# Kernel optimization log

Measured on AMD Instinct MI355X. Metric: run time of the kernel, lower is better.

The kernel has to match this reference:

```python
import jax, jax.numpy as jnp
import numpy as np

D_MODEL = 1024

def setup_inputs() -> dict:
    key = jax.random.key(0)
    ks = jax.random.split(key, 5)
    s = 1.0 / np.sqrt(D_MODEL)  # torch Linear default init scale-ish
    x = jax.random.normal(ks[0], (4, 2048, D_MODEL), dtype=jnp.float32)
    Wq = jax.random.normal(ks[1], (D_MODEL, D_MODEL), dtype=jnp.float32) * s
    Wk = jax.random.normal(ks[2], (D_MODEL, D_MODEL), dtype=jnp.float32) * s
    Wv = jax.random.normal(ks[3], (D_MODEL, D_MODEL), dtype=jnp.float32) * s
    Wo = jax.random.normal(ks[4], (D_MODEL, D_MODEL), dtype=jnp.float32) * s
    z = jnp.zeros((D_MODEL,), dtype=jnp.float32)
    return {"x": x, "Wq": Wq, "bq": z, "Wk": Wk, "bk": z, "Wv": Wv, "bv": z, "Wo": Wo, "bo": z}

def reference(x, Wq, bq, Wk, bk, Wv, bv, Wo, bo):
    # x: (B, S, D). Single-head causal attention, dropout in eval mode (identity).
    B, S, D = x.shape
    Q = jnp.einsum('bsd,ed->bse', x, Wq) + bq
    K = jnp.einsum('bsd,ed->bse', x, Wk) + bk
    V = jnp.einsum('bsd,ed->bse', x, Wv) + bv
    scores = jnp.einsum('bqd,bkd->bqk', Q, K) / jnp.sqrt(jnp.float32(D))
    causal = jnp.tril(jnp.ones((S, S), dtype=bool))  # (S, S)
    scores = jnp.where(causal, scores, -jnp.inf)
    weights = jax.nn.softmax(scores, axis=-1)
    attended = jnp.einsum('bqk,bkd->bqd', weights, V)
    out = jnp.einsum('bsd,ed->bse', attended, Wo) + bo
    return out
```

## Files before the change

### kernel.cpp

```cpp
#include <hip/hip_runtime.h>
#include <cstdint>
#include <cstddef>


#define D_MODEL 1024
#define SEQ     2048
#define BATCH   4

typedef unsigned short u16;
typedef __bf16 bf16_t;
typedef bf16_t bf16x8 __attribute__((ext_vector_type(8)));
typedef float  f32x4  __attribute__((ext_vector_type(4)));
typedef u16    u16x4  __attribute__((ext_vector_type(4)));

__device__ __forceinline__ u16 f2bf(float x) {
  union { float f; uint32_t u; } v; v.f = x;
  uint32_t r = v.u + 0x7fffu + ((v.u >> 16) & 1u);
  return (u16)(r >> 16);
}
__device__ __forceinline__ float bf2f(u16 h) {
  union { uint32_t u; float f; } v; v.u = (uint32_t)h << 16;
  return v.f;
}

__device__ __forceinline__ void gload_lds16(const u16* g, u16* l) {
  __builtin_amdgcn_global_load_lds((__attribute__((address_space(1))) void*)g,
                                   (__attribute__((address_space(3))) void*)l,
                                   16, 0, 0);
}

__device__ __forceinline__ void gemm256(const u16* __restrict__ A,
                                        const u16* __restrict__ B,
                                        int lda, int ldb, int nt64,
                                        u16* As, u16* Bs,
                                        f32x4 acc[8][4]) {
  const int tid  = threadIdx.x;
  const int lane = tid & 63, wave = tid >> 6;
  const int frow = lane & 15, kc = lane >> 4;
  const int abase = (wave >> 2) * 128, bbase = (wave & 3) * 64;
  const int r0 = tid >> 2;
  const int k0 = ((tid & 3) ^ ((r0 >> 1) & 3)) * 8;
  const u16* Arow0 = A + (size_t)r0 * lda + k0;
  const u16* Arow1 = A + (size_t)(r0 + 128) * lda + k0;
  const u16* Brow0 = B + (size_t)r0 * ldb + k0;
  const u16* Brow1 = B + (size_t)(r0 + 128) * ldb + k0;
  int aoff[8], boff[4];
#pragma unroll
  for (int i = 0; i < 8; ++i) {
    const int ra = abase + i * 16 + frow;
    aoff[i] = (ra * 4 + (kc ^ ((ra >> 1) & 3))) * 8;
  }
#pragma unroll
  for (int j = 0; j < 4; ++j) {
    const int rb = bbase + j * 16 + frow;
    boff[j] = (rb * 4 + (kc ^ ((rb >> 1) & 3))) * 8;
  }
  auto stage = [&](int t) {
    u16* ab = As + (t & 1) * 16384;
    u16* bb = Bs + (t & 1) * 16384;
    const int kb = t * 64;
    gload_lds16(Arow0 + kb,      ab + tid * 8);
    gload_lds16(Arow1 + kb,      ab + 4096 + tid * 8);
    gload_lds16(Arow0 + kb + 32, ab + 8192 + tid * 8);
    gload_lds16(Arow1 + kb + 32, ab + 12288 + tid * 8);
    gload_lds16(Brow0 + kb,      bb + tid * 8);
    gload_lds16(Brow1 + kb,      bb + 4096 + tid * 8);
    gload_lds16(Brow0 + kb + 32, bb + 8192 + tid * 8);
    gload_lds16(Brow1 + kb + 32, bb + 12288 + tid * 8);
  };
  stage(0);
  for (int t = 0; t < nt64; ++t) {
    __builtin_amdgcn_s_barrier();
    if (t + 1 < nt64) {
      stage(t + 1);
      asm volatile("s_waitcnt vmcnt(8)" ::: "memory");
    } else {
      asm volatile("s_waitcnt vmcnt(0)" ::: "memory");
    }
    __builtin_amdgcn_s_barrier();
    const u16* ab = As + (t & 1) * 16384;
    const u16* bb = Bs + (t & 1) * 16384;
    bf16x8 a0[4], a1[4], b0[4], b1[4];
#pragma unroll
    for (int j = 0; j < 4; ++j) b0[j] = *(const bf16x8*)(bb + boff[j]);
#pragma unroll
    for (int i = 0; i < 4; ++i) a0[i] = *(const bf16x8*)(ab + aoff[i]);
#pragma unroll
    for (int i = 0; i < 4; ++i) a1[i] = *(const bf16x8*)(ab + aoff[4 + i]);
    __builtin_amdgcn_s_setprio(1);
#pragma unroll
    for (int i = 0; i < 4; ++i)
#pragma unroll
      for (int j = 0; j < 4; ++j)
        acc[i][j] = __builtin_amdgcn_mfma_f32_16x16x32_bf16(a0[i], b0[j], acc[i][j], 0, 0, 0);
    __builtin_amdgcn_s_setprio(0);
#pragma unroll
    for (int j = 0; j < 4; ++j) b1[j] = *(const bf16x8*)(bb + 8192 + boff[j]);
#pragma unroll
    for (int i = 0; i < 4; ++i) a0[i] = *(const bf16x8*)(ab + 8192 + aoff[i]);
    __builtin_amdgcn_s_setprio(1);
#pragma unroll
    for (int i = 0; i < 4; ++i)
#pragma unroll
      for (int j = 0; j < 4; ++j)
        acc[4 + i][j] = __builtin_amdgcn_mfma_f32_16x16x32_bf16(a1[i], b0[j], acc[4 + i][j], 0, 0, 0);
    __builtin_amdgcn_s_setprio(0);
#pragma unroll
    for (int i = 0; i < 4; ++i) a1[i] = *(const bf16x8*)(ab + 8192 + aoff[4 + i]);
    __builtin_amdgcn_s_setprio(1);
#pragma unroll
    for (int i = 0; i < 4; ++i)
#pragma unroll
      for (int j = 0; j < 4; ++j)
        acc[i][j] = __builtin_amdgcn_mfma_f32_16x16x32_bf16(a0[i], b1[j], acc[i][j], 0, 0, 0);
#pragma unroll
    for (int i = 0; i < 4; ++i)
#pragma unroll
      for (int j = 0; j < 4; ++j)
        acc[4 + i][j] = __builtin_amdgcn_mfma_f32_16x16x32_bf16(a1[i], b1[j], acc[4 + i][j], 0, 0, 0);
    __builtin_amdgcn_s_setprio(0);
  }
}

__device__ __forceinline__ void gemm128(const u16* __restrict__ A,
                                        const u16* __restrict__ B,
                                        int lda, int ldb, int nt,
                                        u16* As, u16* Bs,
                                        f32x4 acc[4][2]) {
  const int tid  = threadIdx.x;
  const int lane = tid & 63, wave = tid >> 6;
  const int frow = lane & 15, kc = lane >> 4;
  const int abase = (wave >> 2) * 64, bbase = (wave & 3) * 32;
  const int r0 = tid >> 2;
  const int k0 = ((tid & 3) ^ ((r0 >> 1) & 3)) * 8;
  const u16* Asrc = A + (size_t)r0 * lda + k0;
  const u16* Bsrc = B + (size_t)r0 * ldb + k0;
  int aoff[4], boff[2];
#pragma unroll
  for (int i = 0; i < 4; ++i) {
    const int ra = abase + i * 16 + frow;
    aoff[i] = (ra * 4 + (kc ^ ((ra >> 1) & 3))) * 8;
  }
#pragma unroll
  for (int j = 0; j < 2; ++j) {
    const int rb = bbase + j * 16 + frow;
    boff[j] = (rb * 4 + (kc ^ ((rb >> 1) & 3))) * 8;
  }
  auto stage = [&](int t) {
    u16* ab = As + (t & 3) * 4096;
    u16* bb = Bs + (t & 3) * 4096;
    const int kb = t * 32;
    gload_lds16(Asrc + kb, ab + tid * 8);
    gload_lds16(Bsrc + kb, bb + tid * 8);
  };
  stage(0);
  if (nt > 1) stage(1);
  if (nt > 2) stage(2);
  for (int t = 0; t < nt; ++t) {
    if (t + 2 < nt)      asm volatile("s_waitcnt vmcnt(4)" ::: "memory");
    else if (t + 1 < nt) asm volatile("s_waitcnt vmcnt(2)" ::: "memory");
    else                 asm volatile("s_waitcnt vmcnt(0)" ::: "memory");
    __builtin_amdgcn_s_barrier();
    asm volatile("" ::: "memory");
    if (t + 3 < nt) stage(t + 3);
    const u16* ab = As + (t & 3) * 4096;
    const u16* bb = Bs + (t & 3) * 4096;
    bf16x8 af[4], bf[2];
#pragma unroll
    for (int j = 0; j < 2; ++j) bf[j] = *(const bf16x8*)(bb + boff[j]);
#pragma unroll
    for (int i = 0; i < 4; ++i) af[i] = *(const bf16x8*)(ab + aoff[i]);
    __builtin_amdgcn_s_setprio(1);
#pragma unroll
    for (int i = 0; i < 4; ++i)
#pragma unroll
      for (int j = 0; j < 2; ++j)
        acc[i][j] = __builtin_amdgcn_mfma_f32_16x16x32_bf16(af[i], bf[j], acc[i][j], 0, 0, 0);
    __builtin_amdgcn_s_setprio(0);
    asm volatile("" ::: "memory");
  }
}

__global__ __launch_bounds__(256) void cvt_kernel(const float4* __restrict__ x,
                                                  const float4* __restrict__ wq,
                                                  const float4* __restrict__ wk,
                                                  const float4* __restrict__ wv,
                                                  const float4* __restrict__ wo,
                                                  u16* __restrict__ dst) {
  const int i = blockIdx.x * 256 + threadIdx.x;
  float4 v;
  if (i < 2097152) {
    v = x[i];
  } else {
    const int j = i - 2097152;
    const int w = j >> 18;
    const float4* s = (w == 0) ? wq : (w == 1) ? wk : (w == 2) ? wv : wo;
    v = s[j & 262143];
  }
  u16x4 o = {f2bf(v.x), f2bf(v.y), f2bf(v.z), f2bf(v.w)};
  *(u16x4*)(dst + (size_t)i * 4) = o;
}

__global__ void transposeW_kernel(const u16* __restrict__ src, u16* __restrict__ dst) {
  __shared__ u16 tile[32][33];
  const int r0 = blockIdx.x * 32, c0 = blockIdx.y * 32;
  const int tx = threadIdx.x, ty = threadIdx.y;
#pragma unroll
  for (int r = 0; r < 4; ++r)
    tile[ty + r * 8][tx] = src[(size_t)(r0 + ty + r * 8) * D_MODEL + c0 + tx];
  __syncthreads();
#pragma unroll
  for (int r = 0; r < 4; ++r)
    dst[(size_t)(c0 + ty + r * 8) * D_MODEL + r0 + tx] = tile[tx][ty + r * 8];
}

__global__ __launch_bounds__(512, 2) void stageA_kernel(
    const u16* __restrict__ xb,
    const u16* __restrict__ WqB, const u16* __restrict__ WkB,
    const u16* __restrict__ WoB, const u16* __restrict__ WvT,
    const float* __restrict__ Wo32, const float* __restrict__ bv,
    const float* __restrict__ bq, const float* __restrict__ bk,
    u16* __restrict__ Qb, u16* __restrict__ Kb,
    u16* __restrict__ Wp, float* __restrict__ bp) {
  __shared__ __align__(16) u16 As[32768];
  __shared__ __align__(16) u16 Bs[32768];
  const int blk = blockIdx.x, tid = threadIdx.x;
  const int lane = tid & 63, wave = tid >> 6;
  const int cl = lane & 15, rl = (lane >> 4) * 4;

  if (blk < 256) {
    const int c = blk & 7, i = blk >> 3;
    const int z = i >> 4, w = i & 15;
    const int rt = c * 4 + (w >> 2), ct = w & 3;
    const int row0 = rt * 256, col0 = ct * 256;
    const u16*   W    = z ? WkB : WqB;
    const float* bias = z ? bk : bq;
    u16*         out  = z ? Kb : Qb;
    f32x4 acc[8][4] = {};
    gemm256(xb + (size_t)row0 * D_MODEL, W + (size_t)col0 * D_MODEL,
            D_MODEL, D_MODEL, 16, As, Bs, acc);
    const int abase = (wave >> 2) * 128, bbase = (wave & 3) * 64;
#pragma unroll
    for (int j = 0; j < 4; ++j) {
      const int col = col0 + bbase + j * 16 + cl;
      const float bb = bias[col];
#pragma unroll
      for (int ii = 0; ii < 8; ++ii)
#pragma unroll
        for (int r = 0; r < 4; ++r) {
          const int row = row0 + abase + ii * 16 + rl + r;
          out[(size_t)row * D_MODEL + col] = f2bf(acc[ii][j][r] + bb);
        }
    }
  } else if (blk < 320) {
    const int qq = blk - 256;
    const int t16 = qq >> 2, quad = qq & 3;
    const int f0 = (t16 >> 2) * 256 + (quad >> 1) * 128;
    const int e0 = (t16 & 3) * 256 + (quad & 1) * 128;
    f32x4 acc[4][2] = {};
    gemm128(WoB + (size_t)f0 * D_MODEL, WvT + (size_t)e0 * D_MODEL,
            D_MODEL, D_MODEL, 32, As, Bs, acc);
    const int abase = (wave >> 2) * 64, bbase = (wave & 3) * 32;
#pragma unroll
    for (int j = 0; j < 2; ++j) {
      const int col = e0 + bbase + j * 16 + cl;
#pragma unroll
      for (int ii = 0; ii < 4; ++ii)
#pragma unroll
        for (int r = 0; r < 4; ++r) {
          const int row = f0 + abase + ii * 16 + rl + r;
          Wp[(size_t)row * D_MODEL + col] = f2bf(acc[ii][j][r]);
        }
    }
  } else {
    const int f  = (blk - 320) * 64 + (tid >> 3);
    const int dq = tid & 7;
    const float* row = Wo32 + (size_t)f * D_MODEL + dq * 128;
    const float* bvq = bv + dq * 128;
    float s = 0.f;
#pragma unroll 8
    for (int k = 0; k < 128; ++k) s += row[k] * bvq[k];
    s += __shfl_xor(s, 1);
    s += __shfl_xor(s, 2);
    s += __shfl_xor(s, 4);
    if (dq == 0) bp[f] = s;
  }
}

__global__ __launch_bounds__(512, 2) void stageB_kernel(
    const u16* __restrict__ xb, const u16* __restrict__ Wp,
    const float* __restrict__ bp,
    const u16* __restrict__ Qb, const u16* __restrict__ Kb,
    u16* __restrict__ Vt, u16* __restrict__ Eb, float* __restrict__ rssum) {
  __shared__ __align__(16) u16 As[32768];
  __shared__ __align__(16) u16 Bs[32768];
  const int blk = blockIdx.x, tid = threadIdx.x;
  const int lane = tid & 63, wave = tid >> 6;
  const int cl = lane & 15, rl = (lane >> 4) * 4;

  if (blk < 144) {
    const int c = blk & 7, u = blk >> 3;
    const int b = c >> 1, h = c & 1;
    int qi, ji;
    if (h == 0) {
      if (u < 1)       { qi = 0; ji = u; }
      else if (u < 5)  { qi = 3; ji = u - 1; }
      else if (u < 10) { qi = 4; ji = u - 5; }
      else             { qi = 7; ji = u - 10; }
    } else {
      if (u < 2)       { qi = 1; ji = u; }
      else if (u < 5)  { qi = 2; ji = u - 2; }
      else if (u < 11) { qi = 5; ji = u - 5; }
      else             { qi = 6; ji = u - 11; }
    }
    const u16* A  = Qb + (size_t)(b * SEQ + qi * 256) * D_MODEL;
    const u16* Bt = Kb + (size_t)(b * SEQ + ji * 256) * D_MODEL;
    f32x4 acc[8][4] = {};
    gemm256(A, Bt, D_MODEL, D_MODEL, 16, As, Bs, acc);
    u16* outp = Eb + (size_t)b * SEQ * SEQ;
    float* rs = rssum + b * SEQ;
    const int abase = (wave >> 2) * 128, bbase = (wave & 3) * 64;
#pragma unroll
    for (int ii = 0; ii < 8; ++ii)
#pragma unroll
      for (int r = 0; r < 4; ++r) {
        const int q = qi * 256 + abase + ii * 16 + rl + r;
        float ps = 0.f;
#pragma unroll
        for (int j = 0; j < 4; ++j) {
          const int jj = ji * 256 + bbase + j * 16 + cl;
          u16 h16 = 0;
          if (jj <= q) h16 = f2bf(__expf(acc[ii][j][r] * 0.03125f));
          outp[(size_t)q * SEQ + jj] = h16;
          ps += bf2f(h16);
        }
        ps += __shfl_xor(ps, 1);
        ps += __shfl_xor(ps, 2);
        ps += __shfl_xor(ps, 4);
        ps += __shfl_xor(ps, 8);
        if (cl == 0) atomicAdd(&rs[q], ps);
      }
  } else if (blk < 256) {
    const int v = blk - 144;
    const int rt = v >> 2, ct = v & 3;
    const int row0 = rt * 256, col0 = ct * 256;
    f32x4 acc[8][4] = {};
    gemm256(xb + (size_t)row0 * D_MODEL, Wp + (size_t)col0 * D_MODEL,
            D_MODEL, D_MODEL, 16, As, Bs, acc);
    const int b = row0 >> 11;
    u16* vt = Vt + (size_t)b * D_MODEL * SEQ;
    const int abase = (wave >> 2) * 128, bbase = (wave & 3) * 64;
#pragma unroll
    for (int j = 0; j < 4; ++j) {
      const int col = col0 + bbase + j * 16 + cl;
      const float bb = bp[col];
#pragma unroll
      for (int ii = 0; ii < 8; ++ii) {
        const int s0 = (row0 & 2047) + abase + ii * 16 + rl;
        u16x4 o = {f2bf(acc[ii][j][0] + bb), f2bf(acc[ii][j][1] + bb),
                   f2bf(acc[ii][j][2] + bb), f2bf(acc[ii][j][3] + bb)};
        *(u16x4*)(vt + (size_t)col * SEQ + s0) = o;
      }
    }
  } else {
    const int qq = blk - 256;
    const int t16 = qq >> 2, quad = qq & 3;
    const int rt = 28 + (t16 >> 2), ct = t16 & 3;
    const int row0 = rt * 256 + (quad >> 1) * 128;
    const int col0 = ct * 256 + (quad & 1) * 128;
    f32x4 acc[4][2] = {};
    gemm128(xb + (size_t)row0 * D_MODEL, Wp + (size_t)col0 * D_MODEL,
            D_MODEL, D_MODEL, 32, As, Bs, acc);
    const int b = row0 >> 11;
    u16* vt = Vt + (size_t)b * D_MODEL * SEQ;
    const int abase = (wave >> 2) * 64, bbase = (wave & 3) * 32;
#pragma unroll
    for (int j = 0; j < 2; ++j) {
      const int col = col0 + bbase + j * 16 + cl;
      const float bb = bp[col];
#pragma unroll
      for (int ii = 0; ii < 4; ++ii) {
        const int s0 = (row0 & 2047) + abase + ii * 16 + rl;
        u16x4 o = {f2bf(acc[ii][j][0] + bb), f2bf(acc[ii][j][1] + bb),
                   f2bf(acc[ii][j][2] + bb), f2bf(acc[ii][j][3] + bb)};
        *(u16x4*)(vt + (size_t)col * SEQ + s0) = o;
      }
    }
  }
}

__global__ __launch_bounds__(512, 2) void pv_kernel(const u16* __restrict__ Eb,
                                                    const u16* __restrict__ Vt,
                                                    const float* __restrict__ rssum,
                                                    const float* __restrict__ bo,
                                                    float* __restrict__ Out) {
  __shared__ __align__(16) u16 As[32768];
  __shared__ __align__(16) u16 Bs[32768];
  const int blk = blockIdx.x, tid = threadIdx.x;
  const int c = blk & 7, i = blk >> 3;
  const int b  = c >> 1;
  const int dt = (c & 1) * 2 + (i & 1);
  const int qt = i >> 1;
  const u16* A  = Eb + (size_t)b * SEQ * SEQ + (size_t)(qt * 256) * SEQ;
  const u16* Bt = Vt + (size_t)b * D_MODEL * SEQ + (size_t)(dt * 256) * SEQ;
  f32x4 acc[8][4] = {};
  gemm256(A, Bt, SEQ, SEQ, (qt + 1) * 4, As, Bs, acc);
  const int lane = tid & 63, wave = tid >> 6;
  const int abase = (wave >> 2) * 128, bbase = (wave & 3) * 64;
  const int cl = lane & 15, rl = (lane >> 4) * 4;
#pragma unroll
  for (int ii = 0; ii < 8; ++ii)
#pragma unroll
    for (int r = 0; r < 4; ++r) {
      const int q = qt * 256 + abase + ii * 16 + rl + r;
      const float invl = 1.0f / rssum[b * SEQ + q];
#pragma unroll
      for (int j = 0; j < 4; ++j) {
        const int col = dt * 256 + bbase + j * 16 + cl;
        Out[(size_t)(b * SEQ + q) * D_MODEL + col] = acc[ii][j][r] * invl + bo[col];
      }
    }
}

extern "C" void kernel_launch(void* const* d_in, const int* in_sizes, int n_in,
                              void* d_out, int out_size, void* d_ws, size_t ws_size,
                              hipStream_t stream) {
  const float* x  = (const float*)d_in[0];
  const float* Wq = (const float*)d_in[1];
  const float* bq = (const float*)d_in[2];
  const float* Wk = (const float*)d_in[3];
  const float* bk = (const float*)d_in[4];
  const float* Wv = (const float*)d_in[5];
  const float* bv = (const float*)d_in[6];
  const float* Wo = (const float*)d_in[7];
  const float* bo = (const float*)d_in[8];
  float* out = (float*)d_out;
  char* ws = (char*)d_ws;

  u16*   xb  = (u16*)(ws);
  u16*   Wb  = (u16*)(ws + (16u << 20));
  u16*   Qb  = (u16*)(ws + (24u << 20));
  u16*   Kb  = (u16*)(ws + (40u << 20));
  u16*   Vt  = (u16*)(ws + (56u << 20));
  u16*   Eb  = (u16*)(ws + (72u << 20));
  u16*   WvT = (u16*)(ws + (104u << 20));
  u16*   Wp  = (u16*)(ws + (106u << 20));
  float* bp  = (float*)(ws + (108u << 20));
  float* rssum = (float*)(ws + (20u << 20));

  cvt_kernel<<<12288, 256, 0, stream>>>((const float4*)x, (const float4*)Wq,
                                        (const float4*)Wk, (const float4*)Wv,
                                        (const float4*)Wo, xb);
  transposeW_kernel<<<dim3(32, 32), dim3(32, 8), 0, stream>>>(Wb + (2u << 20), WvT);
  stageA_kernel<<<336, 512, 0, stream>>>(xb, Wb, Wb + (1u << 20), Wb + (3u << 20),
                                         WvT, Wo, bv, bq, bk, Qb, Kb, Wp, bp);
  hipMemsetAsync(rssum, 0, BATCH * SEQ * sizeof(float), stream);
  stageB_kernel<<<320, 512, 0, stream>>>(xb, Wp, bp, Qb, Kb, Vt, Eb, rssum);
  pv_kernel<<<128, 512, 0, stream>>>(Eb, Vt, rssum, bo, out);
}
```

Baseline: 292.3 us.

## Deepen gemm pipeline to 4-stage half-K ring and rebalance PV with paired causal tiles

The shared gemm256 loop moves from a double-buffered 64-wide K step to a 4-deep ring of 32-wide K stages. Loads for stage h+3 are issued between the LDS fragment reads and the MFMAs, and vmcnt waits are tracked per stage, so global latency is hidden further ahead. The PV kernel now uses a new 128x128 gemm with the same ring and 256 blocks. Each block handles a pair of causal query tiles (q and 15-q), giving every block the same total work and filling more CUs. The cost is more barriers per K step and smaller tiles with less operand reuse.

After: 254.3 us. 1.15x faster.

```diff
diff --git a/kernel.cpp b/kernel.cpp
--- a/kernel.cpp
+++ b/kernel.cpp
@@ -55,70 +55,131 @@
     const int rb = bbase + j * 16 + frow;
     boff[j] = (rb * 4 + (kc ^ ((rb >> 1) & 3))) * 8;
   }
-  auto stage = [&](int t) {
-    u16* ab = As + (t & 1) * 16384;
-    u16* bb = Bs + (t & 1) * 16384;
-    const int kb = t * 64;
-    gload_lds16(Arow0 + kb,      ab + tid * 8);
-    gload_lds16(Arow1 + kb,      ab + 4096 + tid * 8);
-    gload_lds16(Arow0 + kb + 32, ab + 8192 + tid * 8);
-    gload_lds16(Arow1 + kb + 32, ab + 12288 + tid * 8);
-    gload_lds16(Brow0 + kb,      bb + tid * 8);
-    gload_lds16(Brow1 + kb,      bb + 4096 + tid * 8);
-    gload_lds16(Brow0 + kb + 32, bb + 8192 + tid * 8);
-    gload_lds16(Brow1 + kb + 32, bb + 12288 + tid * 8);
+  const int H = nt64 * 2;
+  auto stgA = [&](int hh) {
+    const int koff = hh * 32;
+    u16* ab = As + (hh & 3) * 8192;
+    gload_lds16(Arow0 + koff, ab + tid * 8);
+    gload_lds16(Arow1 + koff, ab + 4096 + tid * 8);
   };
-  stage(0);
-  for (int t = 0; t < nt64; ++t) {
-    __builtin_amdgcn_s_barrier();
-    if (t + 1 < nt64) {
-      stage(t + 1);
-      asm volatile("s_waitcnt vmcnt(8)" ::: "memory");
-    } else {
-      asm volatile("s_waitcnt vmcnt(0)" ::: "memory");
-    }
-    __builtin_amdgcn_s_barrier();
-    const u16* ab = As + (t & 1) * 16384;
-    const u16* bb = Bs + (t & 1) * 16384;
-    bf16x8 a0[4], a1[4], b0[4], b1[4];
-#pragma unroll
-    for (int j = 0; j < 4; ++j) b0[j] = *(const bf16x8*)(bb + boff[j]);
-#pragma unroll
-    for (int i = 0; i < 4; ++i) a0[i] = *(const bf16x8*)(ab + aoff[i]);
-#pragma unroll
-    for (int i = 0; i < 4; ++i) a1[i] = *(const bf16x8*)(ab + aoff[4 + i]);
+  auto stgB = [&](int hh) {
+    const int koff = hh * 32;
+    u16* bb = Bs + (hh & 3) * 8192;
+    gload_lds16(Brow0 + koff, bb + tid * 8);
+    gload_lds16(Brow1 + koff, bb + 4096 + tid * 8);
+  };
+  stgA(0); stgB(0);
+  if (H > 1) { stgA(1); stgB(1); }
+  if (H > 2) { stgA(2); stgB(2); }
+  if (H > 2)      asm volatile("s_waitcnt vmcnt(8)" ::: "memory");
+  else if (H > 1) asm volatile("s_waitcnt vmcnt(4)" ::: "memory");
+  else            asm volatile("s_waitcnt vmcnt(0)" ::: "memory");
+  __builtin_amdgcn_s_barrier();
+  for (int h = 0; h < H; ++h) {
+    const u16* ab = As + (h & 3) * 8192;
+    const u16* bb = Bs + (h & 3) * 8192;
+    bf16x8 bf[4], af[4];
+#pragma unroll
+    for (int j = 0; j < 4; ++j) bf[j] = *(const bf16x8*)(bb + boff[j]);
+#pragma unroll
+    for (int i = 0; i < 4; ++i) af[i] = *(const bf16x8*)(ab + aoff[i]);
+    if (h + 3 < H) stgA(h + 3);
+    __builtin_amdgcn_s_barrier();
+    asm volatile("s_waitcnt lgkmcnt(0)" ::: "memory");
+    __builtin_amdgcn_sched_barrier(0);
     __builtin_amdgcn_s_setprio(1);
 #pragma unroll
     for (int i = 0; i < 4; ++i)
 #pragma unroll
       for (int j = 0; j < 4; ++j)
-        acc[i][j] = __builtin_amdgcn_mfma_f32_16x16x32_bf16(a0[i], b0[j], acc[i][j], 0, 0, 0);
+        acc[i][j] = __builtin_amdgcn_mfma_f32_16x16x32_bf16(af[i], bf[j], acc[i][j], 0, 0, 0);
     __builtin_amdgcn_s_setprio(0);
-#pragma unroll
-    for (int j = 0; j < 4; ++j) b1[j] = *(const bf16x8*)(bb + 8192 + boff[j]);
-#pragma unroll
-    for (int i = 0; i < 4; ++i) a0[i] = *(const bf16x8*)(ab + 8192 + aoff[i]);
+    __builtin_amdgcn_s_barrier();
+#pragma unroll
+    for (int i = 0; i < 4; ++i) af[i] = *(const bf16x8*)(ab + aoff[4 + i]);
+    if (h + 3 < H) stgB(h + 3);
+    __builtin_amdgcn_s_barrier();
+    asm volatile("s_waitcnt lgkmcnt(0)" ::: "memory");
+    __builtin_amdgcn_sched_barrier(0);
     __builtin_amdgcn_s_setprio(1);
 #pragma unroll
     for (int i = 0; i < 4; ++i)
 #pragma unroll
       for (int j = 0; j < 4; ++j)
-        acc[4 + i][j] = __builtin_amdgcn_mfma_f32_16x16x32_bf16(a1[i], b0[j], acc[4 + i][j], 0, 0, 0);
+        acc[4 + i][j] = __builtin_amdgcn_mfma_f32_16x16x32_bf16(af[i], bf[j], acc[4 + i][j], 0, 0, 0);
     __builtin_amdgcn_s_setprio(0);
-#pragma unroll
-    for (int i = 0; i < 4; ++i) a1[i] = *(const bf16x8*)(ab + 8192 + aoff[4 + i]);
+    if (h + 1 < H) {
+      const int infl = H - 2 - h;
+      if (infl >= 2)      asm volatile("s_waitcnt vmcnt(8)" ::: "memory");
+      else if (infl == 1) asm volatile("s_waitcnt vmcnt(4)" ::: "memory");
+      else                asm volatile("s_waitcnt vmcnt(0)" ::: "memory");
+    }
+    __builtin_amdgcn_s_barrier();
+  }
+}
+
+__device__ __forceinline__ void gemm128pv(const u16* __restrict__ A,
+                                          const u16* __restrict__ B,
+                                          int lda, int ldb, int H,
+                                          u16* As, u16* Bs,
+                                          f32x4 acc[4][2]) {
+  const int tid  = threadIdx.x;
+  const int lane = tid & 63, wave = tid >> 6;
+  const int frow = lane & 15, kc = lane >> 4;
+  const int abase = (wave >> 2) * 64, bbase = (wave & 3) * 32;
+  const int r0 = tid >> 2;
+  const int k0 = ((tid & 3) ^ ((r0 >> 1) & 3)) * 8;
+  const u16* Asrc = A + (size_t)r0 * lda + k0;
+  const u16* Bsrc = B + (size_t)r0 * ldb + k0;
+  int aoff[4], boff[2];
+#pragma unroll
+  for (int i = 0; i < 4; ++i) {
+    const int ra = abase + i * 16 + frow;
+    aoff[i] = (ra * 4 + (kc ^ ((ra >> 1) & 3))) * 8;
+  }
+#pragma unroll
+  for (int j = 0; j < 2; ++j) {
+    const int rb = bbase + j * 16 + frow;
+    boff[j] = (rb * 4 + (kc ^ ((rb >> 1) & 3))) * 8;
+  }
+  auto stg = [&](int hh) {
+    const int koff = hh * 32;
+    gload_lds16(Asrc + koff, As + (hh & 3) * 4096 + tid * 8);
+    gload_lds16(Bsrc + koff, Bs + (hh & 3) * 4096 + tid * 8);
+  };
+  stg(0);
+  if (H > 1) stg(1);
+  if (H > 2) stg(2);
+  if (H > 2)      asm volatile("s_waitcnt vmcnt(4)" ::: "memory");
+  else if (H > 1) asm volatile("s_waitcnt vmcnt(2)" ::: "memory");
+  else            asm volatile("s_waitcnt vmcnt(0)" ::: "memory");
+  __builtin_amdgcn_s_barrier();
+  for (int h = 0; h < H; ++h) {
+    const u16* ab = As + (h & 3) * 4096;
+    const u16* bb = Bs + (h & 3) * 4096;
+    bf16x8 af[4], bf[2];
+#pragma unroll
+    for (int j = 0; j < 2; ++j) bf[j] = *(const bf16x8*)(bb + boff[j]);
+#pragma unroll
+    for (int i = 0; i < 4; ++i) af[i] = *(const bf16x8*)(ab + aoff[i]);
+    if (h + 3 < H) stg(h + 3);
+    __builtin_amdgcn_s_barrier();
+    asm volatile("s_waitcnt lgkmcnt(0)" ::: "memory");
+    __builtin_amdgcn_sched_barrier(0);
     __builtin_amdgcn_s_setprio(1);
 #pragma unroll
     for (int i = 0; i < 4; ++i)
 #pragma unroll
-      for (int j = 0; j < 4; ++j)
-        acc[i][j] = __builtin_amdgcn_mfma_f32_16x16x32_bf16(a0[i], b1[j], acc[i][j], 0, 0, 0);
-#pragma unroll
-    for (int i = 0; i < 4; ++i)
-#pragma unroll
-      for (int j = 0; j < 4; ++j)
-        acc[4 + i][j] = __builtin_amdgcn_mfma_f32_16x16x32_bf16(a1[i], b1[j], acc[4 + i][j], 0, 0, 0);
+      for (int j = 0; j < 2; ++j)
+        acc[i][j] = __builtin_amdgcn_mfma_f32_16x16x32_bf16(af[i], bf[j], acc[i][j], 0, 0, 0);
     __builtin_amdgcn_s_setprio(0);
+    if (h + 1 < H) {
+      const int infl = H - 2 - h;
+      if (infl >= 2)      asm volatile("s_waitcnt vmcnt(4)" ::: "memory");
+      else if (infl == 1) asm volatile("s_waitcnt vmcnt(2)" ::: "memory");
+      else                asm volatile("s_waitcnt vmcnt(0)" ::: "memory");
+    }
+    __builtin_amdgcn_s_barrier();
   }
 }
 
@@ -394,32 +455,37 @@
                                                     const float* __restrict__ rssum,
                                                     const float* __restrict__ bo,
                                                     float* __restrict__ Out) {
-  __shared__ __align__(16) u16 As[32768];
-  __shared__ __align__(16) u16 Bs[32768];
+  __shared__ __align__(16) u16 As[16384];
+  __shared__ __align__(16) u16 Bs[16384];
   const int blk = blockIdx.x, tid = threadIdx.x;
-  const int c = blk & 7, i = blk >> 3;
+  const int c = blk & 7, s = blk >> 3;
   const int b  = c >> 1;
-  const int dt = (c & 1) * 2 + (i & 1);
-  const int qt = i >> 1;
-  const u16* A  = Eb + (size_t)b * SEQ * SEQ + (size_t)(qt * 256) * SEQ;
-  const u16* Bt = Vt + (size_t)b * D_MODEL * SEQ + (size_t)(dt * 256) * SEQ;
-  f32x4 acc[8][4] = {};
-  gemm256(A, Bt, SEQ, SEQ, (qt + 1) * 4, As, Bs, acc);
+  const int dt8 = (c & 1) * 4 + (s & 3);
+  const int q   = s >> 2;
   const int lane = tid & 63, wave = tid >> 6;
-  const int abase = (wave >> 2) * 128, bbase = (wave & 3) * 64;
+  const int abase = (wave >> 2) * 64, bbase = (wave & 3) * 32;
   const int cl = lane & 15, rl = (lane >> 4) * 4;
-#pragma unroll
-  for (int ii = 0; ii < 8; ++ii)
-#pragma unroll
-    for (int r = 0; r < 4; ++r) {
-      const int q = qt * 256 + abase + ii * 16 + rl + r;
-      const float invl = 1.0f / rssum[b * SEQ + q];
-#pragma unroll
-      for (int j = 0; j < 4; ++j) {
-        const int col = dt * 256 + bbase + j * 16 + cl;
-        Out[(size_t)(b * SEQ + q) * D_MODEL + col] = acc[ii][j][r] * invl + bo[col];
+  const u16* Bt = Vt + (size_t)b * D_MODEL * SEQ + (size_t)(dt8 * 128) * SEQ;
+#pragma unroll 1
+  for (int u = 0; u < 2; ++u) {
+    const int qt = u ? (15 - q) : q;
+    const u16* A = Eb + (size_t)b * SEQ * SEQ + (size_t)(qt * 128) * SEQ;
+    f32x4 acc[4][2] = {};
+    gemm128pv(A, Bt, SEQ, SEQ, (qt + 1) * 4, As, Bs, acc);
+#pragma unroll
+    for (int ii = 0; ii < 4; ++ii)
+#pragma unroll
+      for (int r = 0; r < 4; ++r) {
+        const int qq = qt * 128 + abase + ii * 16 + rl + r;
+        const float invl = 1.0f / rssum[b * SEQ + qq];
+#pragma unroll
+        for (int j = 0; j < 2; ++j) {
+          const int col = dt8 * 128 + bbase + j * 16 + cl;
+          Out[(size_t)(b * SEQ + qq) * D_MODEL + col] = acc[ii][j][r] * invl + bo[col];
+        }
       }
-    }
+    __builtin_amdgcn_s_barrier();
+  }
 }
 
 extern "C" void kernel_launch(void* const* d_in, const int* in_sizes, int n_in,
@@ -456,5 +522,5 @@
                                          WvT, Wo, bv, bq, bk, Qb, Kb, Wp, bp);
   hipMemsetAsync(rssum, 0, BATCH * SEQ * sizeof(float), stream);
   stageB_kernel<<<320, 512, 0, stream>>>(xb, Wp, bp, Qb, Kb, Vt, Eb, rssum);
-  pv_kernel<<<128, 512, 0, stream>>>(Eb, Vt, rssum, bo, out);
-}
+  pv_kernel<<<256, 512, 0, stream>>>(Eb, Vt, rssum, bo, out);
+}
```
